# Performance work log

Measured on AMD Instinct MI355X. Metric: run time of the kernel, lower is better.

Reference implementation:

```python
import jax, jax.numpy as jnp
import numpy as np
from jax import lax

QBITS = 8  # per layer_configs: 8-bit weights and activations


def fake_quant(x, bits=QBITS):
    """Per-tensor symmetric fake quantization with straight-through estimator."""
    qmax = float(2 ** (bits - 1) - 1)  # 127 for 8-bit
    scale = jnp.maximum(jnp.max(jnp.abs(x)), 1e-8) / qmax
    q = jnp.clip(jnp.round(x / scale), -qmax - 1.0, qmax) * scale
    # STE: forward uses q, backward passes gradient through unchanged
    return x + lax.stop_gradient(q - x)


def qconv(x, w, b):
    """Fake-quantized conv: quantize activations and weights, then VALID conv + bias."""
    xq = fake_quant(x)
    wq = fake_quant(w)
    y = lax.conv_general_dilated(
        xq, wq, window_strides=(1, 1), padding='VALID',
        dimension_numbers=('NCHW', 'OIHW', 'NCHW'))
    return y + b[None, :, None, None]


def setup_inputs() -> dict:
    key = jax.random.key(0)
    ks = jax.random.split(key, 9)
    return {
        'x':  jax.random.uniform(ks[0], (256, 1, 128, 128), dtype=jnp.float32),
        'w1': jax.random.normal(ks[1], (16, 1, 3, 3), dtype=jnp.float32) * 0.3,
        'b1': jax.random.normal(ks[2], (16,), dtype=jnp.float32) * 0.05,
        'w2': jax.random.normal(ks[3], (16, 16, 3, 3), dtype=jnp.float32) * 0.1,
        'b2': jax.random.normal(ks[4], (16,), dtype=jnp.float32) * 0.05,
        'w3': jax.random.normal(ks[5], (16, 16, 3, 3), dtype=jnp.float32) * 0.1,
        'b3': jax.random.normal(ks[6], (16,), dtype=jnp.float32) * 0.05,
        'w4': jax.random.normal(ks[7], (1, 16, 2, 2), dtype=jnp.float32) * 0.1,
        'b4': jax.random.normal(ks[8], (1,), dtype=jnp.float32) * 0.05,
    }


def reference(x, w1, b1, w2, b2, w3, b3, w4, b4):
    # x: [N,1,128,128] -> [N,16,126,126] -> [N,16,124,124] -> [N,16,122,122] -> [N,1,121,121]
    h = jax.nn.relu(qconv(x, w1, b1))
    h = jax.nn.relu(qconv(h, w2, b2))
    h = jax.nn.relu(qconv(h, w3, b3))
    return jax.nn.sigmoid(qconv(h, w4, b4))
```

## Files before the change

kernel.cpp:

```cpp
#include <hip/hip_runtime.h>
#include <math.h>


#define THREADS 256

typedef __attribute__((ext_vector_type(4))) int i32x4;

__device__ __forceinline__ int xcd_swz(int bid, int nwg) {
    return (bid & 7) * (nwg >> 3) + (bid >> 3);
}
__device__ __forceinline__ int swzb(int rec) {
    return (rec << 4) ^ ((rec & 56) << 1);
}

__device__ __forceinline__ float block_reduce_max(float m, float* wred) {
#pragma unroll
    for (int off = 32; off > 0; off >>= 1)
        m = fmaxf(m, __shfl_down(m, off, 64));
    if ((threadIdx.x & 63) == 0) wred[threadIdx.x >> 6] = m;
    __syncthreads();
    return fmaxf(fmaxf(wred[0], wred[1]), fmaxf(wred[2], wred[3]));
}

__global__ void init_kernel(unsigned int* slots) {
    if (threadIdx.x < 8) slots[threadIdx.x] = 0u;
}

__global__ void fill_kernel(float* out, int n, float v) {
    int i = blockIdx.x * blockDim.x + threadIdx.x;
    int stride = gridDim.x * blockDim.x;
    for (; i < n; i += stride) out[i] = v;
}

__global__ __launch_bounds__(THREADS) void absmax4_kernel(
    const float4* __restrict__ x, int n4, unsigned int* __restrict__ slot) {
    __shared__ float wred[4];
    float m = 0.f;
    const int stride = gridDim.x * blockDim.x;
    for (int i = blockIdx.x * blockDim.x + threadIdx.x; i < n4; i += stride) {
        float4 v = x[i];
        m = fmaxf(fmaxf(fabsf(v.x), fabsf(v.y)),
                  fmaxf(fmaxf(fabsf(v.z), fabsf(v.w)), m));
    }
    m = block_reduce_max(m, wred);
    if (threadIdx.x == 0) atomicMax(slot, __float_as_uint(m));
}

__global__ __launch_bounds__(THREADS) void quant_w_kernel(
    const float* __restrict__ w1, const float* __restrict__ w2,
    const float* __restrict__ w3, const float* __restrict__ w4,
    float* __restrict__ qw1, float* __restrict__ qw4,
    signed char* __restrict__ wi8_2, signed char* __restrict__ wi8_3,
    unsigned int* __restrict__ slots) {
    __shared__ float wred[4];
    const float* w; int nel;
    switch (blockIdx.x) {
        case 0:  w = w1; nel = 144;  break;
        case 1:  w = w2; nel = 2304; break;
        case 2:  w = w3; nel = 2304; break;
        default: w = w4; nel = 64;   break;
    }
    float m = 0.f;
    for (int i = threadIdx.x; i < nel; i += blockDim.x)
        m = fmaxf(m, fabsf(w[i]));
    m = block_reduce_max(m, wred);
    if (threadIdx.x == 0) slots[4 + blockIdx.x] = __float_as_uint(m);
    const float s = fmaxf(m, 1e-8f) / 127.0f;

    if (blockIdx.x == 0) {
        for (int i = threadIdx.x; i < 144; i += blockDim.x) {
            int p = i % 9, o = i / 9;
            float q = fminf(fmaxf(rintf(w[i] / s), -128.f), 127.f);
            qw1[p * 16 + o] = q * s;
        }
    } else if (blockIdx.x == 3) {
        for (int i = threadIdx.x; i < 64; i += blockDim.x) {
            float q = fminf(fmaxf(rintf(w[i] / s), -128.f), 127.f);
            qw4[i] = q * s;
        }
    } else {
        signed char* wi8 = (blockIdx.x == 1) ? wi8_2 : wi8_3;
        for (int i = threadIdx.x; i < 3072; i += blockDim.x) {
            int ci = i & 15, lane = (i >> 4) & 63, g = i >> 10;
            int co = lane & 15, qq = lane >> 4;
            int pos = 4 * g + qq;
            float v = 0.f;
            if (pos < 9) {
                int ky = pos / 3, kx = pos % 3;
                v = fminf(fmaxf(rintf(w[((co * 16 + ci) * 3 + ky) * 3 + kx] / s),
                                -128.f), 127.f);
            }
            wi8[i] = (signed char)(int)v;
        }
    }
}

__global__ __launch_bounds__(THREADS) void conv1max_kernel(
    const float* __restrict__ x, const float* __restrict__ qw,
    const float* __restrict__ bias, unsigned int* __restrict__ slots) {
    constexpr int IH = 128, IW = 128, OH = 126, OW = 126;
    __shared__ float tile[34 * 34];
    __shared__ float wred[4];
    const int bid = xcd_swz(blockIdx.x, gridDim.x);
    const int n = bid >> 4, tr = bid & 15;
    const int oy0 = (tr >> 2) * 32, ox0 = (tr & 3) * 32;
    const float s_in = fmaxf(__uint_as_float(slots[0]), 1e-8f) / 127.0f;
    const float* xN = x + (size_t)n * IH * IW;

#pragma unroll
    for (int it = 0; it < 5; ++it) {
        int px = it * 256 + threadIdx.x;
        if (px < 1156) {
            int iy = px / 34, ix = px - iy * 34;
            int gy = min(oy0 + iy, IH - 1), gx = min(ox0 + ix, IW - 1);
            float q = rintf(xN[gy * IW + gx] / s_in);
            tile[px] = fminf(fmaxf(q, -128.f), 127.f);
        }
    }
    __syncthreads();

    const int tx = (threadIdx.x & 15) * 2, ty = (threadIdx.x >> 4) * 2;
    float p[4][4];
#pragma unroll
    for (int r = 0; r < 4; ++r) {
        const float* rp = &tile[(ty + r) * 34 + tx];
        p[r][0] = rp[0]; p[r][1] = rp[1]; p[r][2] = rp[2]; p[r][3] = rp[3];
    }
    float accm[16];
#pragma unroll
    for (int c = 0; c < 16; ++c) accm[c] = -3.0e38f;

#pragma unroll
    for (int sy = 0; sy < 2; ++sy)
#pragma unroll
    for (int sx = 0; sx < 2; ++sx) {
        float acc[16];
#pragma unroll
        for (int c = 0; c < 16; ++c) acc[c] = 0.f;
#pragma unroll
        for (int ky = 0; ky < 3; ++ky)
#pragma unroll
        for (int kx = 0; kx < 3; ++kx) {
            const float xv = p[sy + ky][sx + kx];
            const float* wp = qw + (ky * 3 + kx) * 16;
#pragma unroll
            for (int co = 0; co < 16; ++co)
                acc[co] = fmaf(xv, wp[co], acc[co]);
        }
        const int oy = oy0 + ty + sy, ox = ox0 + tx + sx;
        if (oy < OH && ox < OW) {
#pragma unroll
            for (int co = 0; co < 16; ++co)
                accm[co] = fmaxf(accm[co], acc[co]);
        }
    }
    float m = 0.f;
#pragma unroll
    for (int co = 0; co < 16; ++co)
        m = fmaxf(m, fmaxf(fmaf(accm[co], s_in, bias[co]), 0.f));
    m = block_reduce_max(m, wred);
    if (threadIdx.x == 0) atomicMax(&slots[1], __float_as_uint(m));
}

__global__ __launch_bounds__(THREADS) void k3_kernel(
    const float* __restrict__ x, const float* __restrict__ qw1,
    const float* __restrict__ b1, signed char* __restrict__ h1out,
    const signed char* __restrict__ wi8_2, const float* __restrict__ b2,
    unsigned int* __restrict__ slots) {
    __shared__ float xt[36 * 36];
    __shared__ signed char h1t[34 * 34 * 16 + 128];
    __shared__ float wred[4];
    const int bid = xcd_swz(blockIdx.x, gridDim.x);
    const int n = bid / 25, tr = bid % 25;
    const int ty = (tr / 5) * 30, tx = (tr % 5) * 30;
    const int tid = threadIdx.x;

    const float s_x = fmaxf(__uint_as_float(slots[0]), 1e-8f) / 127.0f;
    const float r1  = 127.0f / fmaxf(__uint_as_float(slots[1]), 1e-8f);
    const float* xN = x + (size_t)n * 128 * 128;

    for (int i = tid; i < 1296; i += THREADS) {
        int iy = i / 36, ix = i - iy * 36;
        int gy = min(ty + iy, 127), gx = min(tx + ix, 127);
        float q = rintf(xN[gy * 128 + gx] / s_x);
        xt[i] = fminf(fmaxf(q, -128.f), 127.f);
    }
    __syncthreads();

    for (int p = tid; p < 1156; p += THREADS) {
        int py = p / 34, px = p - py * 34;
        float acc[16];
#pragma unroll
        for (int c = 0; c < 16; ++c) acc[c] = 0.f;
#pragma unroll
        for (int ky = 0; ky < 3; ++ky)
#pragma unroll
        for (int kx = 0; kx < 3; ++kx) {
            const float xv = xt[(py + ky) * 36 + px + kx];
            const float* wp = qw1 + (ky * 3 + kx) * 16;
#pragma unroll
            for (int co = 0; co < 16; ++co)
                acc[co] = fmaf(xv, wp[co], acc[co]);
        }
        unsigned pk[4] = {0u, 0u, 0u, 0u};
#pragma unroll
        for (int co = 0; co < 16; ++co) {
            float y = fmaxf(fmaf(acc[co], s_x, b1[co]), 0.f);
            float q8 = fminf(rintf(y * r1), 127.f);
            pk[co >> 2] |= ((unsigned)(int)q8) << ((co & 3) * 8);
        }
        int4 v; v.x = pk[0]; v.y = pk[1]; v.z = pk[2]; v.w = pk[3];
        *(int4*)(h1t + swzb(p)) = v;
        const int gy = ty + py, gx = tx + px;
        if (gy <= 125 && gx <= 125)
            *(int4*)(h1out + ((size_t)(n * 126 + gy) * 126 + gx) * 16) = v;
    }

    i32x4 afrag[3];
#pragma unroll
    for (int g = 0; g < 3; ++g)
        afrag[g] = ((const i32x4*)wi8_2)[g * 64 + (tid & 63)];
    __syncthreads();

    const int lane = tid & 63, wv = tid >> 6;
    const int q = lane >> 4, col = lane & 15;
    const int wr = wv >> 1, wc = wv & 1;
    int drec[3];
#pragma unroll
    for (int g = 0; g < 3; ++g) {
        int pos = 4 * g + q;
        int dy = (pos < 9) ? pos / 3 : 0;
        int dx = (pos < 9) ? pos % 3 : 0;
        drec[g] = dy * 34 + dx;
    }
    const int ix2 = 16 * wc + col;
    int mi[4];
#pragma unroll
    for (int j = 0; j < 4; ++j) mi[j] = INT_MIN;

#pragma unroll 4
    for (int r = 0; r < 16; ++r) {
        const int iy2 = 16 * wr + r;
        const int rec = iy2 * 34 + ix2;
        i32x4 acc = {0, 0, 0, 0};
#pragma unroll
        for (int g = 0; g < 3; ++g) {
            i32x4 b = *(const i32x4*)(h1t + swzb(rec + drec[g]));
            acc = __builtin_amdgcn_mfma_i32_16x16x64_i8(afrag[g], b, acc, 0, 0, 0);
        }
        if (ty + iy2 <= 123 && tx + ix2 <= 123) {
#pragma unroll
            for (int j = 0; j < 4; ++j)
                mi[j] = (acc[j] > mi[j]) ? acc[j] : mi[j];
        }
    }
    const float s1  = fmaxf(__uint_as_float(slots[1]), 1e-8f) / 127.0f;
    const float sw2 = fmaxf(__uint_as_float(slots[5]), 1e-8f) / 127.0f;
    const float sxw = s1 * sw2;
    float m = 0.f;
#pragma unroll
    for (int j = 0; j < 4; ++j)
        m = fmaxf(m, fmaxf(fmaf((float)mi[j], sxw, b2[q * 4 + j]), 0.f));
    m = block_reduce_max(m, wred);
    if (tid == 0) atomicMax(&slots[2], __float_as_uint(m));
}

__global__ __launch_bounds__(THREADS) void k4_kernel(
    const signed char* __restrict__ h1, const signed char* __restrict__ wi8_2,
    const float* __restrict__ b2, signed char* __restrict__ h2out,
    const signed char* __restrict__ wi8_3, const float* __restrict__ b3,
    unsigned int* __restrict__ slots) {
    __shared__ signed char h1t[34 * 34 * 16 + 128];
    __shared__ signed char h2t[32 * 32 * 16 + 128];
    __shared__ float wred[4];
    const int bid = xcd_swz(blockIdx.x, gridDim.x);
    const int n = bid / 25, tr = bid % 25;
    const int ty = (tr / 5) * 30, tx = (tr % 5) * 30;
    const int tid = threadIdx.x, lane = tid & 63, wv = tid >> 6;
    const int q = lane >> 4, col = lane & 15;
    const int wr = wv >> 1, wc = wv & 1;

    const signed char* h1N = h1 + (size_t)n * 126 * 126 * 16;
#pragma unroll
    for (int it = 0; it < 5; ++it) {
        int p = it * 256 + tid;
        if (p < 1156) {
            int iy = p / 34, ix = p - iy * 34;
            int gy = min(ty + iy, 125), gx = min(tx + ix, 125);
            *(int4*)(h1t + swzb(p)) =
                *(const int4*)(h1N + ((size_t)gy * 126 + gx) * 16);
        }
    }
    i32x4 af2[3], af3[3];
#pragma unroll
    for (int g = 0; g < 3; ++g) {
        af2[g] = ((const i32x4*)wi8_2)[g * 64 + lane];
        af3[g] = ((const i32x4*)wi8_3)[g * 64 + lane];
    }
    __syncthreads();

    int d34[3], d32[3];
#pragma unroll
    for (int g = 0; g < 3; ++g) {
        int pos = 4 * g + q;
        int dy = (pos < 9) ? pos / 3 : 0;
        int dx = (pos < 9) ? pos % 3 : 0;
        d34[g] = dy * 34 + dx;
        d32[g] = dy * 32 + dx;
    }
    const float s1  = fmaxf(__uint_as_float(slots[1]), 1e-8f) / 127.0f;
    const float sw2 = fmaxf(__uint_as_float(slots[5]), 1e-8f) / 127.0f;
    const float sxw2 = s1 * sw2;
    const float r2 = 127.0f / fmaxf(__uint_as_float(slots[2]), 1e-8f);
    float b2j[4];
#pragma unroll
    for (int j = 0; j < 4; ++j) b2j[j] = b2[q * 4 + j];

    const int ix2 = 16 * wc + col;
    signed char* h2N = h2out + (size_t)n * 124 * 124 * 16;

#pragma unroll 4
    for (int r = 0; r < 16; ++r) {
        const int iy2 = 16 * wr + r;
        const int rec = iy2 * 34 + ix2;
        i32x4 acc = {0, 0, 0, 0};
#pragma unroll
        for (int g = 0; g < 3; ++g) {
            i32x4 b = *(const i32x4*)(h1t + swzb(rec + d34[g]));
            acc = __builtin_amdgcn_mfma_i32_16x16x64_i8(af2[g], b, acc, 0, 0, 0);
        }
        unsigned pk = 0u;
#pragma unroll
        for (int j = 0; j < 4; ++j) {
            float y = fmaxf(fmaf((float)acc[j], sxw2, b2j[j]), 0.f);
            float q8 = fminf(rintf(y * r2), 127.f);
            pk |= ((unsigned)(int)q8) << (j * 8);
        }
        *(unsigned*)(h2t + swzb(iy2 * 32 + ix2) + q * 4) = pk;
        const int gy = ty + iy2, gx = tx + ix2;
        if (gy <= 123 && gx <= 123)
            *(unsigned*)(h2N + ((size_t)gy * 124 + gx) * 16 + q * 4) = pk;
    }
    __syncthreads();

    int mi[4];
#pragma unroll
    for (int j = 0; j < 4; ++j) mi[j] = INT_MIN;
#pragma unroll 4
    for (int r = 0; r < 16; ++r) {
        const int iy3 = 16 * wr + r;
        if (iy3 <= 29) {
            const int rec = iy3 * 32 + ix2;
            i32x4 acc = {0, 0, 0, 0};
#pragma unroll
            for (int g = 0; g < 3; ++g) {
                i32x4 b = *(const i32x4*)(h2t + swzb(rec + d32[g]));
                acc = __builtin_amdgcn_mfma_i32_16x16x64_i8(af3[g], b, acc, 0, 0, 0);
            }
            if (ix2 <= 29 && ty + iy3 <= 121 && tx + ix2 <= 121) {
#pragma unroll
                for (int j = 0; j < 4; ++j)
                    mi[j] = (acc[j] > mi[j]) ? acc[j] : mi[j];
            }
        }
    }
    const float s2  = fmaxf(__uint_as_float(slots[2]), 1e-8f) / 127.0f;
    const float sw3 = fmaxf(__uint_as_float(slots[6]), 1e-8f) / 127.0f;
    const float sxw3 = s2 * sw3;
    float m = 0.f;
#pragma unroll
    for (int j = 0; j < 4; ++j)
        m = fmaxf(m, fmaxf(fmaf((float)mi[j], sxw3, b3[q * 4 + j]), 0.f));
    m = block_reduce_max(m, wred);
    if (tid == 0) atomicMax(&slots[3], __float_as_uint(m));
}

__global__ __launch_bounds__(THREADS) void k5_kernel(
    const signed char* __restrict__ h2, const signed char* __restrict__ wi8_3,
    const float* __restrict__ b3, const float* __restrict__ qw4,
    const float* __restrict__ b4, float* __restrict__ out,
    unsigned int* __restrict__ slots) {
    __shared__ signed char h2t[34 * 34 * 16 + 128];
    __shared__ signed char h3t[32 * 32 * 16 + 128];
    const int bid = xcd_swz(blockIdx.x, gridDim.x);
    const int n = bid / 25, tr = bid % 25;
    const int ty = (tr / 5) * 30, tx = (tr % 5) * 30;
    const int tid = threadIdx.x, lane = tid & 63, wv = tid >> 6;
    const int q = lane >> 4, col = lane & 15;
    const int wr = wv >> 1, wc = wv & 1;

    const signed char* h2N = h2 + (size_t)n * 124 * 124 * 16;
#pragma unroll
    for (int it = 0; it < 5; ++it) {
        int p = it * 256 + tid;
        if (p < 1156) {
            int iy = p / 34, ix = p - iy * 34;
            int gy = min(ty + iy, 123), gx = min(tx + ix, 123);
            *(int4*)(h2t + swzb(p)) =
                *(const int4*)(h2N + ((size_t)gy * 124 + gx) * 16);
        }
    }
    i32x4 af3[3];
#pragma unroll
    for (int g = 0; g < 3; ++g)
        af3[g] = ((const i32x4*)wi8_3)[g * 64 + lane];
    __syncthreads();

    int d34[3];
#pragma unroll
    for (int g = 0; g < 3; ++g) {
        int pos = 4 * g + q;
        int dy = (pos < 9) ? pos / 3 : 0;
        int dx = (pos < 9) ? pos % 3 : 0;
        d34[g] = dy * 34 + dx;
    }
    const float s2  = fmaxf(__uint_as_float(slots[2]), 1e-8f) / 127.0f;
    const float sw3 = fmaxf(__uint_as_float(slots[6]), 1e-8f) / 127.0f;
    const float sxw3 = s2 * sw3;
    const float r3 = 127.0f / fmaxf(__uint_as_float(slots[3]), 1e-8f);
    float b3j[4];
#pragma unroll
    for (int j = 0; j < 4; ++j) b3j[j] = b3[q * 4 + j];
    const int ix3 = 16 * wc + col;

#pragma unroll 4
    for (int r = 0; r < 16; ++r) {
        const int iy3 = 16 * wr + r;
        const int rec = iy3 * 34 + ix3;
        i32x4 acc = {0, 0, 0, 0};
#pragma unroll
        for (int g = 0; g < 3; ++g) {
            i32x4 b = *(const i32x4*)(h2t + swzb(rec + d34[g]));
            acc = __builtin_amdgcn_mfma_i32_16x16x64_i8(af3[g], b, acc, 0, 0, 0);
        }
        unsigned pk = 0u;
#pragma unroll
        for (int j = 0; j < 4; ++j) {
            float y = fmaxf(fmaf((float)acc[j], sxw3, b3j[j]), 0.f);
            float q8 = fminf(rintf(y * r3), 127.f);
            pk |= ((unsigned)(int)q8) << (j * 8);
        }
        *(unsigned*)(h3t + swzb(iy3 * 32 + ix3) + q * 4) = pk;
    }
    __syncthreads();

    const float s3 = fmaxf(__uint_as_float(slots[3]), 1e-8f) / 127.0f;
    const float bb = b4[0];
    float w[64];
#pragma unroll
    for (int i = 0; i < 64; ++i) w[i] = qw4[i];
    float* outN = out + (size_t)n * 121 * 121;

#pragma unroll
    for (int it = 0; it < 4; ++it) {
        int p = it * 256 + tid;
        if (p < 961) {
            int r = p / 31, c = p - r * 31;
            float acc = 0.f;
#pragma unroll
            for (int ky = 0; ky < 2; ++ky)
#pragma unroll
            for (int kx = 0; kx < 2; ++kx) {
                union { int4 v; signed char ch[16]; } u;
                u.v = *(const int4*)(h3t + swzb((r + ky) * 32 + (c + kx)));
#pragma unroll
                for (int ci = 0; ci < 16; ++ci)
                    acc = fmaf((float)u.ch[ci], w[(ci * 2 + ky) * 2 + kx], acc);
            }
            const int gy = ty + r, gx = tx + c;
            if (gy <= 120 && gx <= 120) {
                float y = fmaf(acc, s3, bb);
                outN[(size_t)gy * 121 + gx] = 1.0f / (1.0f + expf(-y));
            }
        }
    }
}

extern "C" void kernel_launch(void* const* d_in, const int* in_sizes, int n_in,
                              void* d_out, int out_size, void* d_ws, size_t ws_size,
                              hipStream_t stream) {
    (void)in_sizes; (void)n_in;
    const float* x  = (const float*)d_in[0];
    const float* w1 = (const float*)d_in[1];
    const float* b1 = (const float*)d_in[2];
    const float* w2 = (const float*)d_in[3];
    const float* b2 = (const float*)d_in[4];
    const float* w3 = (const float*)d_in[5];
    const float* b3 = (const float*)d_in[6];
    const float* w4 = (const float*)d_in[7];
    const float* b4 = (const float*)d_in[8];

    char* ws = (char*)d_ws;
    unsigned int* slots = (unsigned int*)ws;
    float* qw1 = (float*)(ws + 256);
    float* qw4 = (float*)(ws + 1024);
    signed char* wi8_2 = (signed char*)(ws + 2048);
    signed char* wi8_3 = (signed char*)(ws + 5120);

    const size_t Q1 = 65028096ULL;
    const size_t Q2 = 62980096ULL;
    signed char* qb1 = (signed char*)(ws + 32768);
    signed char* qb2 = (signed char*)(ws + 32768 + Q1);
    float* outp = (float*)d_out;

    const size_t need = 32768ULL + Q1 + Q2;
    if (ws_size < need) {
        float v = 100.0f + (float)(ws_size >> 20);
        hipLaunchKernelGGL(fill_kernel, dim3(1024), dim3(THREADS), 0, stream,
                           outp, out_size, v);
        return;
    }

    hipLaunchKernelGGL(init_kernel, dim3(1), dim3(64), 0, stream, slots);
    hipLaunchKernelGGL(absmax4_kernel, dim3(2048), dim3(THREADS), 0, stream,
                       (const float4*)x, 256 * 128 * 128 / 4, slots + 0);
    hipLaunchKernelGGL(quant_w_kernel, dim3(4), dim3(THREADS), 0, stream,
                       w1, w2, w3, w4, qw1, qw4, wi8_2, wi8_3, slots);

    hipLaunchKernelGGL(conv1max_kernel, dim3(256 * 16), dim3(THREADS), 0, stream,
                       x, qw1, b1, slots);
    const int fgrid = 256 * 25;
    hipLaunchKernelGGL(k3_kernel, dim3(fgrid), dim3(THREADS), 0, stream,
                       x, qw1, b1, qb1, wi8_2, b2, slots);
    hipLaunchKernelGGL(k4_kernel, dim3(fgrid), dim3(THREADS), 0, stream,
                       qb1, wi8_2, b2, qb2, wi8_3, b3, slots);
    hipLaunchKernelGGL(k5_kernel, dim3(fgrid), dim3(THREADS), 0, stream,
                       qb2, wi8_3, b3, qw4, b4, outp, slots);
}
```

Measured before the change: 363.3 us.

## Compute conv1 inside k3 with int8 MFMA and retile to 32x32 blocks

The first convolution inside the fused k3 kernel is recomputed with an int8 16x16x64 MFMA instead of per-pixel fp32 FMAs over 16 channels. Input pixels are kept as int8 in shared memory, and packed int8 conv1 weights are prepared once in quant_w_kernel. The k3 grid also moves from overlapping 30-stride tiles (25 per image) to non-overlapping 32-stride tiles (16 per image), which cuts redundant halo work. The cost is that most of each MFMA is zero-padded, and the packed window reads touch uninitialized shared bytes, which only multiply zero weights.

After: 311.1 us. 14.4% less time.

```diff
diff --git a/kernel.cpp b/kernel.cpp
--- a/kernel.cpp
+++ b/kernel.cpp
@@ -49,7 +49,7 @@
 __global__ __launch_bounds__(THREADS) void quant_w_kernel(
     const float* __restrict__ w1, const float* __restrict__ w2,
     const float* __restrict__ w3, const float* __restrict__ w4,
-    float* __restrict__ qw1, float* __restrict__ qw4,
+    float* __restrict__ qw1, int* __restrict__ qw1p, float* __restrict__ qw4,
     signed char* __restrict__ wi8_2, signed char* __restrict__ wi8_3,
     unsigned int* __restrict__ slots) {
     __shared__ float wred[4];
@@ -72,6 +72,19 @@
             int p = i % 9, o = i / 9;
             float q = fminf(fmaxf(rintf(w[i] / s), -128.f), 127.f);
             qw1[p * 16 + o] = q * s;
+        }
+        if (threadIdx.x < 64) {
+            int qq = threadIdx.x >> 4, co = threadIdx.x & 15;
+            unsigned pk = 0u;
+            if (qq < 3) {
+#pragma unroll
+                for (int dx = 0; dx < 3; ++dx) {
+                    float qv = fminf(fmaxf(rintf(w[co * 9 + qq * 3 + dx] / s),
+                                           -128.f), 127.f);
+                    pk |= ((unsigned)(int)qv & 0xffu) << (8 * dx);
+                }
+            }
+            qw1p[threadIdx.x] = (int)pk;
         }
     } else if (blockIdx.x == 3) {
         for (int i = threadIdx.x; i < 64; i += blockDim.x) {
@@ -163,67 +176,73 @@
 }
 
 __global__ __launch_bounds__(THREADS) void k3_kernel(
-    const float* __restrict__ x, const float* __restrict__ qw1,
+    const float* __restrict__ x, const int* __restrict__ qw1p,
     const float* __restrict__ b1, signed char* __restrict__ h1out,
     const signed char* __restrict__ wi8_2, const float* __restrict__ b2,
     unsigned int* __restrict__ slots) {
-    __shared__ float xt[36 * 36];
+    __shared__ signed char xq[40 * 40];
     __shared__ signed char h1t[34 * 34 * 16 + 128];
     __shared__ float wred[4];
     const int bid = xcd_swz(blockIdx.x, gridDim.x);
-    const int n = bid / 25, tr = bid % 25;
-    const int ty = (tr / 5) * 30, tx = (tr % 5) * 30;
-    const int tid = threadIdx.x;
-
-    const float s_x = fmaxf(__uint_as_float(slots[0]), 1e-8f) / 127.0f;
-    const float r1  = 127.0f / fmaxf(__uint_as_float(slots[1]), 1e-8f);
+    const int n = bid >> 4, tr = bid & 15;
+    const int ty = (tr >> 2) * 32, tx = (tr & 3) * 32;
+    const int tid = threadIdx.x, lane = tid & 63, wv = tid >> 6;
+    const int q = lane >> 4, col = lane & 15;
+
+    const float s_x  = fmaxf(__uint_as_float(slots[0]), 1e-8f) / 127.0f;
+    const float sw1  = fmaxf(__uint_as_float(slots[4]), 1e-8f) / 127.0f;
+    const float sxw1 = s_x * sw1;
+    const float r1   = 127.0f / fmaxf(__uint_as_float(slots[1]), 1e-8f);
     const float* xN = x + (size_t)n * 128 * 128;
 
     for (int i = tid; i < 1296; i += THREADS) {
         int iy = i / 36, ix = i - iy * 36;
         int gy = min(ty + iy, 127), gx = min(tx + ix, 127);
-        float q = rintf(xN[gy * 128 + gx] / s_x);
-        xt[i] = fminf(fmaxf(q, -128.f), 127.f);
-    }
-    __syncthreads();
-
-    for (int p = tid; p < 1156; p += THREADS) {
-        int py = p / 34, px = p - py * 34;
-        float acc[16];
-#pragma unroll
-        for (int c = 0; c < 16; ++c) acc[c] = 0.f;
-#pragma unroll
-        for (int ky = 0; ky < 3; ++ky)
-#pragma unroll
-        for (int kx = 0; kx < 3; ++kx) {
-            const float xv = xt[(py + ky) * 36 + px + kx];
-            const float* wp = qw1 + (ky * 3 + kx) * 16;
-#pragma unroll
-            for (int co = 0; co < 16; ++co)
-                acc[co] = fmaf(xv, wp[co], acc[co]);
-        }
-        unsigned pk[4] = {0u, 0u, 0u, 0u};
-#pragma unroll
-        for (int co = 0; co < 16; ++co) {
-            float y = fmaxf(fmaf(acc[co], s_x, b1[co]), 0.f);
-            float q8 = fminf(rintf(y * r1), 127.f);
-            pk[co >> 2] |= ((unsigned)(int)q8) << ((co & 3) * 8);
-        }
-        int4 v; v.x = pk[0]; v.y = pk[1]; v.z = pk[2]; v.w = pk[3];
-        *(int4*)(h1t + swzb(p)) = v;
-        const int gy = ty + py, gx = tx + px;
-        if (gy <= 125 && gx <= 125)
-            *(int4*)(h1out + ((size_t)(n * 126 + gy) * 126 + gx) * 16) = v;
-    }
-
-    i32x4 afrag[3];
+        float qf = rintf(xN[gy * 128 + gx] / s_x);
+        qf = fminf(fmaxf(qf, -128.f), 127.f);
+        xq[iy * 40 + ix] = (signed char)(int)qf;
+    }
+
+    i32x4 a1 = {qw1p[q * 16 + col], 0, 0, 0};
+    i32x4 af2[3];
 #pragma unroll
     for (int g = 0; g < 3; ++g)
-        afrag[g] = ((const i32x4*)wi8_2)[g * 64 + (tid & 63)];
-    __syncthreads();
-
-    const int lane = tid & 63, wv = tid >> 6;
-    const int q = lane >> 4, col = lane & 15;
+        af2[g] = ((const i32x4*)wi8_2)[g * 64 + lane];
+    float b1j[4], b2j[4];
+#pragma unroll
+    for (int j = 0; j < 4; ++j) { b1j[j] = b1[q * 4 + j]; b2j[j] = b2[q * 4 + j]; }
+    __syncthreads();
+
+    for (int py = wv; py < 34; py += 4) {
+#pragma unroll
+        for (int g3 = 0; g3 < 3; ++g3) {
+            const int pxx = g3 * 16 + col;
+            const int base = (py + q) * 40 + (pxx & ~3);
+            unsigned lo = *(const unsigned*)(xq + base);
+            unsigned hi = *(const unsigned*)(xq + base + 4);
+            unsigned win = (unsigned)((((unsigned long long)hi << 32) | lo)
+                                      >> ((pxx & 3) * 8));
+            i32x4 b = {(int)win, 0, 0, 0};
+            i32x4 z = {0, 0, 0, 0};
+            i32x4 acc = __builtin_amdgcn_mfma_i32_16x16x64_i8(a1, b, z, 0, 0, 0);
+            if (pxx < 34) {
+                unsigned pk = 0u;
+#pragma unroll
+                for (int j = 0; j < 4; ++j) {
+                    float y = fmaxf(fmaf((float)acc[j], sxw1, b1j[j]), 0.f);
+                    float q8 = fminf(rintf(y * r1), 127.f);
+                    pk |= ((unsigned)(int)q8) << (j * 8);
+                }
+                *(unsigned*)(h1t + swzb(py * 34 + pxx) + q * 4) = pk;
+                const int gy = ty + py, gx = tx + pxx;
+                if (gy <= 125 && gx <= 125)
+                    *(unsigned*)(h1out + ((size_t)(n * 126 + gy) * 126 + gx) * 16
+                                 + q * 4) = pk;
+            }
+        }
+    }
+    __syncthreads();
+
     const int wr = wv >> 1, wc = wv & 1;
     int drec[3];
 #pragma unroll
@@ -246,7 +265,7 @@
 #pragma unroll
         for (int g = 0; g < 3; ++g) {
             i32x4 b = *(const i32x4*)(h1t + swzb(rec + drec[g]));
-            acc = __builtin_amdgcn_mfma_i32_16x16x64_i8(afrag[g], b, acc, 0, 0, 0);
+            acc = __builtin_amdgcn_mfma_i32_16x16x64_i8(af2[g], b, acc, 0, 0, 0);
         }
         if (ty + iy2 <= 123 && tx + ix2 <= 123) {
 #pragma unroll
@@ -260,7 +279,7 @@
     float m = 0.f;
 #pragma unroll
     for (int j = 0; j < 4; ++j)
-        m = fmaxf(m, fmaxf(fmaf((float)mi[j], sxw, b2[q * 4 + j]), 0.f));
+        m = fmaxf(m, fmaxf(fmaf((float)mi[j], sxw, b2j[j]), 0.f));
     m = block_reduce_max(m, wred);
     if (tid == 0) atomicMax(&slots[2], __float_as_uint(m));
 }
@@ -493,7 +512,8 @@
     char* ws = (char*)d_ws;
     unsigned int* slots = (unsigned int*)ws;
     float* qw1 = (float*)(ws + 256);
-    float* qw4 = (float*)(ws + 1024);
+    int*   qw1p = (int*)(ws + 1024);
+    float* qw4 = (float*)(ws + 1536);
     signed char* wi8_2 = (signed char*)(ws + 2048);
     signed char* wi8_3 = (signed char*)(ws + 5120);
 
@@ -515,13 +535,13 @@
     hipLaunchKernelGGL(absmax4_kernel, dim3(2048), dim3(THREADS), 0, stream,
                        (const float4*)x, 256 * 128 * 128 / 4, slots + 0);
     hipLaunchKernelGGL(quant_w_kernel, dim3(4), dim3(THREADS), 0, stream,
-                       w1, w2, w3, w4, qw1, qw4, wi8_2, wi8_3, slots);
+                       w1, w2, w3, w4, qw1, qw1p, qw4, wi8_2, wi8_3, slots);
 
     hipLaunchKernelGGL(conv1max_kernel, dim3(256 * 16), dim3(THREADS), 0, stream,
                        x, qw1, b1, slots);
+    hipLaunchKernelGGL(k3_kernel, dim3(256 * 16), dim3(THREADS), 0, stream,
+                       x, qw1p, b1, qb1, wi8_2, b2, slots);
     const int fgrid = 256 * 25;
-    hipLaunchKernelGGL(k3_kernel, dim3(fgrid), dim3(THREADS), 0, stream,
-                       x, qw1, b1, qb1, wi8_2, b2, slots);
     hipLaunchKernelGGL(k4_kernel, dim3(fgrid), dim3(THREADS), 0, stream,
                        qb1, wi8_2, b2, qb2, wi8_3, b3, slots);
     hipLaunchKernelGGL(k5_kernel, dim3(fgrid), dim3(THREADS), 0, stream,
```
